# Kernel optimization log

Hardware: AMD Instinct MI355X
Metric: run time of the kernel (lower is better)

Reference implementation:

```python
import jax, jax.numpy as jnp
import numpy as np

B, H, S, D = 2, 12, 3456, 32
FEATS_PER_T = 216
WINDOW_LEN = 8
ACT_SIZE = 16
IMG_FEAT_SIZE = 196
DECODER_ONLY = False


def eye_mask(seq_len, feats_per_t, window_len, act_size, img_feat_size, decoder_only=False):
    """Boolean [S, S] mask replicating get_eye_block_mask's memory_mask."""
    idx = jnp.arange(seq_len)
    q_t = (idx // feats_per_t)[:, None]          # [S,1]
    kv_t = (idx // feats_per_t)[None, :]         # [1,S]
    q_m = (idx % feats_per_t)[:, None]
    kv_m = (idx % feats_per_t)[None, :]
    proprio_idx_mod = 2 + 1 + 1
    img_start = feats_per_t - img_feat_size
    joint_start = img_start - act_size

    causal = (q_t >= kv_t) & (q_t - kv_t < window_len)
    is_q_img = q_m >= img_start
    is_kv_img = kv_m >= img_start
    is_q_joint = (q_m >= joint_start) & (q_m < img_start)
    is_kv_joint = (kv_m >= joint_start) & (kv_m < img_start)
    is_kv_proprio = kv_m == proprio_idx_mod

    img_to_img = ~(is_q_img & is_kv_img)
    same_t = q_t == kv_t
    joint_past_joint = ~(is_q_joint & is_kv_joint & ~same_t)
    proprio_past = ~(is_kv_proprio & (kv_t < q_t))
    past_image = ~(is_kv_img & (kv_t < q_t))
    m = causal & img_to_img & joint_past_joint & proprio_past & past_image
    if decoder_only:
        m = m & ~(is_q_img & ~is_kv_img)
    return m


def setup_inputs() -> dict:
    key = jax.random.key(0)
    kq, kk, kv = jax.random.split(key, 3)
    return {
        "q": jax.random.normal(kq, (B, H, S, D), dtype=jnp.float32),
        "k": jax.random.normal(kk, (B, H, S, D), dtype=jnp.float32),
        "v": jax.random.normal(kv, (B, H, S, D), dtype=jnp.float32),
        "feats_per_t": FEATS_PER_T,
        "window_len": WINDOW_LEN,
        "act_size": ACT_SIZE,
        "img_feat_size": IMG_FEAT_SIZE,
    }


def reference(q, k, v, feats_per_t, window_len, act_size, img_feat_size):
    seq_len = q.shape[2]
    mask = eye_mask(seq_len, feats_per_t, window_len, act_size,
                    img_feat_size, DECODER_ONLY)  # [S,S]
    scale = 1.0 / jnp.sqrt(jnp.array(q.shape[-1], q.dtype))
    scores = jnp.einsum("bhqd,bhkd->bhqk", q, k) * scale
    neg = jnp.asarray(jnp.finfo(scores.dtype).min, scores.dtype)
    scores = jnp.where(mask[None, None], scores, neg)
    attn = jax.nn.softmax(scores, axis=-1)
    return jnp.einsum("bhqk,bhkd->bhqd", attn, v)
```

## Files before the change

kernel.cpp:

```cpp
#include <hip/hip_runtime.h>

#define SEQ   3456
#define DH    32
#define FPT   216
#define NT    16
#define IMG0  20
#define SCALE 0.17677669529663687f

#define KPAD   40
#define VPAD   168
#define PPITCH 40

typedef __attribute__((ext_vector_type(8))) short bf16x8;
typedef __attribute__((ext_vector_type(4))) float f32x4;

#define MFMA16(a,b,c) __builtin_amdgcn_mfma_f32_16x16x32_bf16(a,b,c,0,0,0)

__device__ __forceinline__ unsigned short bfh(float f) {
    unsigned u = __float_as_uint(f);
    u += 0x7FFFu + ((u >> 16) & 1u);
    return (unsigned short)(u >> 16);
}
__device__ __forceinline__ float bff(unsigned short h) {
    return __uint_as_float((unsigned)h << 16);
}
__device__ __forceinline__ void split8(const float* f, bf16x8& hi, bf16x8& lo) {
    #pragma unroll
    for (int j = 0; j < 8; ++j) {
        unsigned short h = bfh(f[j]);
        hi[j] = (short)h;
        lo[j] = (short)bfh(f[j] - bff(h));
    }
}

__global__ __launch_bounds__(256)
void eye_attn_mfma2(const float* __restrict__ q, const float* __restrict__ k,
                    const float* __restrict__ v, float* __restrict__ out) {
    __shared__ __align__(16) unsigned short KsHi[160 * KPAD];
    __shared__ __align__(16) unsigned short KsLo[160 * KPAD];
    __shared__ __align__(16) unsigned short VtHi[DH * VPAD];
    __shared__ __align__(16) unsigned short Pu[4 * 16 * PPITCH];

    const int t = blockIdx.x, bh = blockIdx.y, half = blockIdx.z;
    const int tid = threadIdx.x;
    const size_t base = (size_t)bh * SEQ * DH;
    const int dmax = (t < 7) ? t : 7;
    const int nkeys = IMG0 * (dmax + 1);

    for (int i = tid; i < 160 * 8; i += 256) {
        const int g = i >> 3, c = i & 7;
        float4 kk = make_float4(0.f,0.f,0.f,0.f), vv = make_float4(0.f,0.f,0.f,0.f);
        if (g < nkeys) {
            const int d = g / IMG0, jj = g - d * IMG0;
            const size_t row = base + (size_t)((t - d) * FPT + jj) * DH + c * 4;
            kk = *(const float4*)(k + row);
            vv = *(const float4*)(v + row);
        }
        const float kf[4] = {kk.x, kk.y, kk.z, kk.w};
        const float vf[4] = {vv.x, vv.y, vv.z, vv.w};
        ushort4 khi, klo;
        unsigned short* ah = (unsigned short*)&khi;
        unsigned short* al = (unsigned short*)&klo;
        #pragma unroll
        for (int e = 0; e < 4; ++e) {
            const unsigned short h = bfh(kf[e]);
            ah[e] = h;
            al[e] = bfh(kf[e] - bff(h));
        }
        *(ushort4*)(KsHi + g * KPAD + c * 4) = khi;
        *(ushort4*)(KsLo + g * KPAD + c * 4) = klo;
        #pragma unroll
        for (int e = 0; e < 4; ++e)
            VtHi[(c * 4 + e) * VPAD + g] = bfh(vf[e]);
    }
    __syncthreads();

    const int wv = tid >> 6, lane = tid & 63;
    const int col = lane & 15, quad = lane >> 4;

    int mt[2]; int mcnt; bool do_img = false;
    if (half == 0) {
        if (wv == 0)      { mt[0] = 0; mcnt = 1; do_img = true; }
        else if (wv == 1) { mt[0] = 1; mcnt = 1; do_img = true; }
        else if (wv == 2) { mt[0] = 2; mt[1] = 3; mcnt = 2; }
        else              { mt[0] = 4; mt[1] = 5; mcnt = 2; }
    } else {
        mt[0] = 6 + 2 * wv; mt[1] = 7 + 2 * wv; mcnt = 2;
    }

    bf16x8 bones;
    #pragma unroll
    for (int j = 0; j < 8; ++j) bones[j] = (short)(col == 0 ? 0x3F80 : 0);

    unsigned short* myP = Pu + wv * 16 * PPITCH;
    const int nkt = (nkeys + 31) >> 5;

    for (int mi = 0; mi < mcnt; ++mi) {
        const int mb = mt[mi] * 16;
        bf16x8 qhi, qlo;
        {
            const int qc = min(mb + col, FPT - 1);
            const float* qp = q + base + (size_t)(t * FPT + qc) * DH + quad * 8;
            float qf[8];
            const float4 a0 = *(const float4*)qp;
            const float4 a1 = *(const float4*)(qp + 4);
            qf[0]=a0.x*SCALE; qf[1]=a0.y*SCALE; qf[2]=a0.z*SCALE; qf[3]=a0.w*SCALE;
            qf[4]=a1.x*SCALE; qf[5]=a1.y*SCALE; qf[6]=a1.z*SCALE; qf[7]=a1.w*SCALE;
            split8(qf, qhi, qlo);
        }
        f32x4 oacc0 = {0.f,0.f,0.f,0.f}, oacc1 = {0.f,0.f,0.f,0.f};
        f32x4 lacc = {0.f,0.f,0.f,0.f};

        for (int kt = 0; kt < nkt; ++kt) {
            f32x4 s[2];
            #pragma unroll
            for (int h = 0; h < 2; ++h) {
                const int key = kt * 32 + h * 16 + col;
                const bf16x8 khi = *(const bf16x8*)(KsHi + key * KPAD + quad * 8);
                const bf16x8 klo = *(const bf16x8*)(KsLo + key * KPAD + quad * 8);
                f32x4 acc = {0.f,0.f,0.f,0.f};
                acc = MFMA16(qhi, khi, acc);
                acc = MFMA16(qlo, khi, acc);
                acc = MFMA16(qhi, klo, acc);
                s[h] = acc;
            }
            #pragma unroll
            for (int h = 0; h < 2; ++h) {
                const int g = kt * 32 + h * 16 + col;
                const int d = g / IMG0, jj = g - d * IMG0;
                #pragma unroll
                for (int r = 0; r < 4; ++r) {
                    const int qm = mb + quad * 4 + r;
                    const bool qj = (qm >= 4) && (qm < IMG0);
                    const bool vis = (g < nkeys) && (qm < FPT) &&
                                     ((d == 0) || ((jj != 4) && !(qj && jj >= 4)));
                    const float e = vis ? __expf(s[h][r]) : 0.f;
                    myP[(quad * 4 + r) * PPITCH + h * 16 + col] = bfh(e);
                }
            }
            const bf16x8 phi = *(const bf16x8*)(myP + col * PPITCH + quad * 8);
            #pragma unroll
            for (int h = 0; h < 2; ++h) {
                const int dim = h * 16 + col;
                const bf16x8 vhi = *(const bf16x8*)(VtHi + dim * VPAD + kt * 32 + quad * 8);
                f32x4& oa = h ? oacc1 : oacc0;
                oa = MFMA16(phi, vhi, oa);
            }
            lacc = MFMA16(phi, bones, lacc);
        }

        if (mi == 0 && do_img) {
            for (int kt2 = 0; kt2 < 7; ++kt2) {
                f32x4 s[2];
                #pragma unroll
                for (int h = 0; h < 2; ++h) {
                    const int keyc = min(IMG0 + kt2 * 32 + h * 16 + col, FPT - 1);
                    const float* kp = k + base + (size_t)(t * FPT + keyc) * DH + quad * 8;
                    float kf[8];
                    const float4 a0 = *(const float4*)kp;
                    const float4 a1 = *(const float4*)(kp + 4);
                    kf[0]=a0.x; kf[1]=a0.y; kf[2]=a0.z; kf[3]=a0.w;
                    kf[4]=a1.x; kf[5]=a1.y; kf[6]=a1.z; kf[7]=a1.w;
                    bf16x8 khi, klo;
                    split8(kf, khi, klo);
                    f32x4 acc = {0.f,0.f,0.f,0.f};
                    acc = MFMA16(qhi, khi, acc);
                    acc = MFMA16(qlo, khi, acc);
                    acc = MFMA16(qhi, klo, acc);
                    s[h] = acc;
                }
                #pragma unroll
                for (int h = 0; h < 2; ++h) {
                    const int key = IMG0 + kt2 * 32 + h * 16 + col;
                    #pragma unroll
                    for (int r = 0; r < 4; ++r) {
                        const int qm = mb + quad * 4 + r;
                        const bool vis = (key < FPT) && (qm < IMG0);
                        const float e = vis ? __expf(s[h][r]) : 0.f;
                        myP[(quad * 4 + r) * PPITCH + h * 16 + col] = bfh(e);
                    }
                }
                const bf16x8 phi = *(const bf16x8*)(myP + col * PPITCH + quad * 8);
                #pragma unroll
                for (int h = 0; h < 2; ++h) {
                    const int dim = h * 16 + col;
                    float vf[8];
                    #pragma unroll
                    for (int j = 0; j < 8; ++j) {
                        const int ky = min(IMG0 + kt2 * 32 + quad * 8 + j, FPT - 1);
                        vf[j] = v[base + (size_t)(t * FPT + ky) * DH + dim];
                    }
                    bf16x8 vhi;
                    #pragma unroll
                    for (int j = 0; j < 8; ++j) vhi[j] = (short)bfh(vf[j]);
                    f32x4& oa = h ? oacc1 : oacc0;
                    oa = MFMA16(phi, vhi, oa);
                }
                lacc = MFMA16(phi, bones, lacc);
            }
        }

        #pragma unroll
        for (int r = 0; r < 4; ++r) {
            const float lr = __shfl(lacc[r], lane & 48);
            const float inv = 1.f / lr;
            const int qm = mb + quad * 4 + r;
            if (qm < FPT) {
                float* op = out + base + (size_t)(t * FPT + qm) * DH;
                op[col]      = oacc0[r] * inv;
                op[16 + col] = oacc1[r] * inv;
            }
        }
    }
}

extern "C" void kernel_launch(void* const* d_in, const int* in_sizes, int n_in,
                              void* d_out, int out_size, void* d_ws, size_t ws_size,
                              hipStream_t stream) {
    const float* q = (const float*)d_in[0];
    const float* k = (const float*)d_in[1];
    const float* v = (const float*)d_in[2];
    float* out = (float*)d_out;
    const int BH = in_sizes[0] / (SEQ * DH);
    dim3 grid(NT, BH, 2);
    eye_attn_mfma2<<<grid, 256, 0, stream>>>(q, k, v, out);
}
```

Measured before the change: 97.72 us.

## Drop K low-part MFMA, use precomputed visibility bitmasks, fully unroll key loop

Removes the K low-bf16 split, which eliminates one of the three MFMAs per score tile along with the KsLo shared buffer and its conversion work. Replaces the per-element visibility arithmetic (division by IMG0 and branches) with per-tile 32-bit bitmasks from constant tables. The main key loop is fully unrolled to 5 tiles, and the P scratch is double-buffered per wave. Score precision drops to a bf16 split on Q only, which risks larger error against the fp32 reference, and the unroll raises register pressure.

```diff
diff --git a/kernel.cpp b/kernel.cpp
--- a/kernel.cpp
+++ b/kernel.cpp
@@ -33,13 +33,17 @@
     }
 }
 
+__constant__ unsigned MN_TAB[5] = {0xFEFFFFFFu, 0xFFFFEFFFu, 0xFFEFFFFEu,
+                                   0xEFFFFEFFu, 0xFFFEFFFFu};
+__constant__ unsigned MJ_TAB[5] = {0x00FFFFFFu, 0xF0000F00u, 0x000F0000u,
+                                   0x0F0000F0u, 0x0000F000u};
+
 __global__ __launch_bounds__(256)
-void eye_attn_mfma2(const float* __restrict__ q, const float* __restrict__ k,
+void eye_attn_mfma3(const float* __restrict__ q, const float* __restrict__ k,
                     const float* __restrict__ v, float* __restrict__ out) {
     __shared__ __align__(16) unsigned short KsHi[160 * KPAD];
-    __shared__ __align__(16) unsigned short KsLo[160 * KPAD];
     __shared__ __align__(16) unsigned short VtHi[DH * VPAD];
-    __shared__ __align__(16) unsigned short Pu[4 * 16 * PPITCH];
+    __shared__ __align__(16) unsigned short Pu[8 * 16 * PPITCH];
 
     const int t = blockIdx.x, bh = blockIdx.y, half = blockIdx.z;
     const int tid = threadIdx.x;
@@ -58,17 +62,11 @@
         }
         const float kf[4] = {kk.x, kk.y, kk.z, kk.w};
         const float vf[4] = {vv.x, vv.y, vv.z, vv.w};
-        ushort4 khi, klo;
+        ushort4 khi;
         unsigned short* ah = (unsigned short*)&khi;
-        unsigned short* al = (unsigned short*)&klo;
-        #pragma unroll
-        for (int e = 0; e < 4; ++e) {
-            const unsigned short h = bfh(kf[e]);
-            ah[e] = h;
-            al[e] = bfh(kf[e] - bff(h));
-        }
+        #pragma unroll
+        for (int e = 0; e < 4; ++e) ah[e] = bfh(kf[e]);
         *(ushort4*)(KsHi + g * KPAD + c * 4) = khi;
-        *(ushort4*)(KsLo + g * KPAD + c * 4) = klo;
         #pragma unroll
         for (int e = 0; e < 4; ++e)
             VtHi[(c * 4 + e) * VPAD + g] = bfh(vf[e]);
@@ -77,6 +75,16 @@
 
     const int wv = tid >> 6, lane = tid & 63;
     const int col = lane & 15, quad = lane >> 4;
+
+    unsigned mNt[5], mJt[5];
+    #pragma unroll
+    for (int kt = 0; kt < 5; ++kt) {
+        const int tr = nkeys - kt * 32;
+        unsigned mn = MN_TAB[kt], mj = MJ_TAB[kt];
+        if (tr <= 0) { mn = 0u; mj = 0u; }
+        else if (tr < 32) { const unsigned lim = (1u << tr) - 1u; mn &= lim; mj &= lim; }
+        mNt[kt] = mn; mJt[kt] = mj;
+    }
 
     int mt[2]; int mcnt; bool do_img = false;
     if (half == 0) {
@@ -91,9 +99,6 @@
     bf16x8 bones;
     #pragma unroll
     for (int j = 0; j < 8; ++j) bones[j] = (short)(col == 0 ? 0x3F80 : 0);
-
-    unsigned short* myP = Pu + wv * 16 * PPITCH;
-    const int nkt = (nkeys + 31) >> 5;
 
     for (int mi = 0; mi < mcnt; ++mi) {
         const int mb = mt[mi] * 16;
@@ -111,30 +116,28 @@
         f32x4 oacc0 = {0.f,0.f,0.f,0.f}, oacc1 = {0.f,0.f,0.f,0.f};
         f32x4 lacc = {0.f,0.f,0.f,0.f};
 
-        for (int kt = 0; kt < nkt; ++kt) {
+        #pragma unroll
+        for (int kt = 0; kt < 5; ++kt) {
+            unsigned short* myP = Pu + (wv * 2 + (kt & 1)) * 16 * PPITCH;
             f32x4 s[2];
             #pragma unroll
             for (int h = 0; h < 2; ++h) {
                 const int key = kt * 32 + h * 16 + col;
                 const bf16x8 khi = *(const bf16x8*)(KsHi + key * KPAD + quad * 8);
-                const bf16x8 klo = *(const bf16x8*)(KsLo + key * KPAD + quad * 8);
                 f32x4 acc = {0.f,0.f,0.f,0.f};
                 acc = MFMA16(qhi, khi, acc);
                 acc = MFMA16(qlo, khi, acc);
-                acc = MFMA16(qhi, klo, acc);
                 s[h] = acc;
             }
             #pragma unroll
-            for (int h = 0; h < 2; ++h) {
-                const int g = kt * 32 + h * 16 + col;
-                const int d = g / IMG0, jj = g - d * IMG0;
-                #pragma unroll
-                for (int r = 0; r < 4; ++r) {
-                    const int qm = mb + quad * 4 + r;
-                    const bool qj = (qm >= 4) && (qm < IMG0);
-                    const bool vis = (g < nkeys) && (qm < FPT) &&
-                                     ((d == 0) || ((jj != 4) && !(qj && jj >= 4)));
-                    const float e = vis ? __expf(s[h][r]) : 0.f;
+            for (int r = 0; r < 4; ++r) {
+                const int qm = mb + quad * 4 + r;
+                const bool isj = (qm >= 4) && (qm < IMG0);
+                const unsigned m = (qm < FPT) ? (isj ? mJt[kt] : mNt[kt]) : 0u;
+                #pragma unroll
+                for (int h = 0; h < 2; ++h) {
+                    const float e = ((m >> (h * 16 + col)) & 1u)
+                                    ? __expf(s[h][r]) : 0.f;
                     myP[(quad * 4 + r) * PPITCH + h * 16 + col] = bfh(e);
                 }
             }
@@ -151,6 +154,7 @@
 
         if (mi == 0 && do_img) {
             for (int kt2 = 0; kt2 < 7; ++kt2) {
+                unsigned short* myP = Pu + (wv * 2 + (kt2 & 1)) * 16 * PPITCH;
                 f32x4 s[2];
                 #pragma unroll
                 for (int h = 0; h < 2; ++h) {
@@ -161,12 +165,12 @@
                     const float4 a1 = *(const float4*)(kp + 4);
                     kf[0]=a0.x; kf[1]=a0.y; kf[2]=a0.z; kf[3]=a0.w;
                     kf[4]=a1.x; kf[5]=a1.y; kf[6]=a1.z; kf[7]=a1.w;
-                    bf16x8 khi, klo;
-                    split8(kf, khi, klo);
+                    bf16x8 khi;
+                    #pragma unroll
+                    for (int j = 0; j < 8; ++j) khi[j] = (short)bfh(kf[j]);
                     f32x4 acc = {0.f,0.f,0.f,0.f};
                     acc = MFMA16(qhi, khi, acc);
                     acc = MFMA16(qlo, khi, acc);
-                    acc = MFMA16(qhi, klo, acc);
                     s[h] = acc;
                 }
                 #pragma unroll
@@ -223,5 +227,5 @@
     float* out = (float*)d_out;
     const int BH = in_sizes[0] / (SEQ * DH);
     dim3 grid(NT, BH, 2);
-    eye_attn_mfma2<<<grid, 256, 0, stream>>>(q, k, v, out);
-}
+    eye_attn_mfma3<<<grid, 256, 0, stream>>>(q, k, v, out);
+}
```

Measured after the change: 100.9 us. 3.3% more time.
